# Kernel tuning notes

Hardware: AMD Instinct MI355X
Metric: run time of the kernel (lower is better)

The kernel has to match this reference:

```python
import jax, jax.numpy as jnp
import numpy as np

B, L, C = 4, 2048, 1024
H = 16
D = C // H  # head_dim = 64


def _rope(t, cos, sin):
    # t: [B, H, L, D]; cos/sin: [L, D//2] broadcast to [1, 1, L, D//2]
    te = t[..., ::2]
    to = t[..., 1::2]
    c = cos[None, None]
    s = sin[None, None]
    re = te * c - to * s
    ro = te * s + to * c
    # interleave even/odd back: [..., D//2, 2] -> [..., D]
    return jnp.stack([re, ro], axis=-1).reshape(t.shape)


def setup_inputs() -> dict:
    key = jax.random.key(0)
    ks = jax.random.split(key, 5)
    x = jax.random.normal(ks[0], (B, L, C), dtype=jnp.float32)
    # rotary phases: theta_i = 10000^(-2i/D), angles = pos * theta
    inv_freq = 1.0 / (10000.0 ** (np.arange(0, D, 2, dtype=np.float32) / D))
    ang = np.arange(L, dtype=np.float32)[:, None] * inv_freq[None, :]  # [L, D//2]
    cos = jnp.asarray(np.cos(ang))
    sin = jnp.asarray(np.sin(ang))
    w_qkv = jax.random.normal(ks[1], (3 * C, C), dtype=jnp.float32) * (C ** -0.5)
    w_proj = jax.random.normal(ks[2], (C, C), dtype=jnp.float32) * (C ** -0.5)
    b_proj = jnp.zeros((C,), dtype=jnp.float32)
    return {"x": x, "cos": cos, "sin": sin, "w_qkv": w_qkv, "w_proj": w_proj, "b_proj": b_proj}


def reference(x, cos, sin, w_qkv, w_proj, b_proj):
    Bx, Lx, Cx = x.shape
    # QKV projection (torch Linear: y = x @ W.T), then split heads
    qkv = jnp.einsum("blc,fc->blf", x, w_qkv)  # [B, L, 3C]
    qkv = qkv.reshape(Bx, Lx, 3, H, D).transpose(2, 0, 3, 1, 4)  # [3, B, H, L, D]
    q, k, v = qkv[0], qkv[1], qkv[2]
    q = _rope(q, cos, sin)
    k = _rope(k, cos, sin)
    # scaled dot-product attention, non-causal
    scale = D ** -0.5
    scores = jnp.einsum("bhqd,bhkd->bhqk", q, k) * scale
    attn = jax.nn.softmax(scores, axis=-1)
    o = jnp.einsum("bhqk,bhkd->bhqd", attn, v)  # [B, H, L, D]
    o = o.transpose(0, 2, 1, 3).reshape(Bx, Lx, Cx)
    return jnp.einsum("blc,fc->blf", o, w_proj) + b_proj
```

## Files before the change

### kernel.cpp

```cpp
#include <hip/hip_runtime.h>
#include <hip/hip_bf16.h>
#include <cstdint>


typedef unsigned short u16;
typedef __attribute__((ext_vector_type(8))) short bf16x8;
typedef __attribute__((ext_vector_type(4))) float f32x4;
typedef __attribute__((ext_vector_type(2))) unsigned int u32x2;

#define GLD16(g, l)                                                            \
  __builtin_amdgcn_global_load_lds(                                            \
      (const __attribute__((address_space(1))) void*)(g),                      \
      (__attribute__((address_space(3))) void*)(l), 16, 0, 0)

static __device__ __forceinline__ u16 f32_bf16(float f) {
  union { float f; unsigned u; } v; v.f = f;
  unsigned r = v.u + 0x7FFFu + ((v.u >> 16) & 1u);
  return (u16)(r >> 16);
}
static __device__ __forceinline__ float bf16_f32(u16 h) {
  union { unsigned u; float f; } v; v.u = ((unsigned)h) << 16;
  return v.f;
}
static __device__ __forceinline__ unsigned pack_rne(float a, float b) {
  union { float f; unsigned u; } x, y; x.f = a; y.f = b;
  unsigned ua = x.u + 0x7FFFu + ((x.u >> 16) & 1u);
  unsigned ub = y.u + 0x7FFFu + ((y.u >> 16) & 1u);
  return (ua >> 16) | (ub & 0xFFFF0000u);
}
static __device__ __forceinline__ unsigned pack_bf16_hw(float a, float b) {
  float2 t; t.x = a; t.y = b;
  __hip_bfloat162 h = __float22bfloat162_rn(t);
  union { __hip_bfloat162 h; unsigned u; } c; c.h = h;
  return c.u;
}

__global__ __launch_bounds__(256) void convert_all(
    const void* __restrict__ x, const void* __restrict__ wq,
    const void* __restrict__ wp, const void* __restrict__ cs,
    const void* __restrict__ sn, const void* __restrict__ bs,
    u16* __restrict__ xb, u16* __restrict__ wqb, u16* __restrict__ wpb,
    u16* __restrict__ cb, u16* __restrict__ sb, u16* __restrict__ bb) {
  const unsigned f32mode = (((const unsigned*)cs)[0] == 0x3F800000u);
  int blk = blockIdx.x;
  if (blk >= 12288 && blk < 12416) {
    const void* src = (blk < 12352) ? cs : sn;
    u16* dst = (blk < 12352) ? cb : sb;
    int i = (blk - ((blk < 12352) ? 12288 : 12352)) * 256 + threadIdx.x;
    u16 e[4];
    if (f32mode) {
      float4 v = ((const float4*)src)[i];
      const float* vf = (const float*)&v;
#pragma unroll
      for (int c = 0; c < 4; c++) e[c] = f32_bf16(vf[c]);
    } else {
      uint2 v = ((const uint2*)src)[i];
      e[0] = (u16)(v.x & 0xFFFFu); e[1] = (u16)(v.x >> 16);
      e[2] = (u16)(v.y & 0xFFFFu); e[3] = (u16)(v.y >> 16);
    }
#pragma unroll
    for (int c = 0; c < 4; c++) {
      int E = i * 4 + c;
      dst[(E & 31) * 2048 + (E >> 5)] = e[c];
    }
    return;
  }
  const void* src; u16* dst; int i0, n4;
  if (blk < 8192)       { src = x;  dst = xb;  i0 = blk;         n4 = 2097152; }
  else if (blk < 11264) { src = wq; dst = wqb; i0 = blk - 8192;  n4 = 786432; }
  else if (blk < 12288) { src = wp; dst = wpb; i0 = blk - 11264; n4 = 262144; }
  else                  { src = bs; dst = bb;  i0 = blk - 12416; n4 = 256; }
  int i = i0 * 256 + threadIdx.x;
  if (i >= n4) return;
  if (f32mode) {
    float4 v = ((const float4*)src)[i];
    uint2 o;
    o.x = pack_rne(v.x, v.y);
    o.y = pack_rne(v.z, v.w);
    ((uint2*)dst)[i] = o;
  } else {
    ((uint2*)dst)[i] = ((const uint2*)src)[i];
  }
}

static __device__ __forceinline__ void gemm_mainloop(
    const u16* __restrict__ A, const u16* __restrict__ Bm, int K,
    int m0, int n0, u16* As, u16* Bs, f32x4 acc[4][4]) {
  const int tid  = threadIdx.x;
  const int lane = tid & 63;
  const int wave = tid >> 6;
  const int n16  = lane & 15;
  const int quad = lane >> 4;
  const int wm = (wave >> 1) * 64;
  const int wn = (wave & 1) * 64;
  const u16* ag = A  + (size_t)(m0 + wave * 16 + (lane >> 2)) * K + (lane & 3) * 8;
  const u16* bg = Bm + (size_t)(n0 + wave * 16 + (lane >> 2)) * K + (lane & 3) * 8;
  u16* al = As + wave * (16 * 32);
  u16* bl = Bs + wave * (16 * 32);
  GLD16(ag, al);
  GLD16(ag + (size_t)64 * K, al + 64 * 32);
  GLD16(bg, bl);
  GLD16(bg + (size_t)64 * K, bl + 64 * 32);
  for (int kt = 0; kt < K; kt += 32) {
    const int buf = (kt >> 5) & 1;
    __syncthreads();
    if (kt + 32 < K) {
      const int nb = buf ^ 1;
      GLD16(ag + kt + 32, al + nb * 4096);
      GLD16(ag + (size_t)64 * K + kt + 32, al + nb * 4096 + 64 * 32);
      GLD16(bg + kt + 32, bl + nb * 4096);
      GLD16(bg + (size_t)64 * K + kt + 32, bl + nb * 4096 + 64 * 32);
    }
    const u16* as = As + buf * 4096;
    const u16* bs = Bs + buf * 4096;
    bf16x8 af[4], bf[4];
#pragma unroll
    for (int i = 0; i < 4; i++)
      af[i] = *(const bf16x8*)(as + (wm + i * 16 + n16) * 32 + quad * 8);
#pragma unroll
    for (int j = 0; j < 4; j++)
      bf[j] = *(const bf16x8*)(bs + (wn + j * 16 + n16) * 32 + quad * 8);
#pragma unroll
    for (int i = 0; i < 4; i++)
#pragma unroll
      for (int j = 0; j < 4; j++)
        acc[i][j] = __builtin_amdgcn_mfma_f32_16x16x32_bf16(af[i], bf[j], acc[i][j], 0, 0, 0);
  }
}

__global__ __launch_bounds__(256) void gemm_qkv(
    const u16* __restrict__ x, const u16* __restrict__ w,
    u16* __restrict__ q_ws, u16* __restrict__ k_ws, u16* __restrict__ vt_ws,
    const u16* __restrict__ cosT, const u16* __restrict__ sinT) {
  __shared__ u16 As[2 * 128 * 32];
  __shared__ u16 Bs[2 * 128 * 32];
  f32x4 acc[4][4];
#pragma unroll
  for (int i = 0; i < 4; i++)
#pragma unroll
    for (int j = 0; j < 4; j++) acc[i][j] = (f32x4){0.f, 0.f, 0.f, 0.f};
  const int m0 = blockIdx.y * 128;
  const int n0 = blockIdx.x * 128;
  gemm_mainloop(x, w, 1024, m0, n0, As, Bs, acc);
  const int lane = threadIdx.x & 63, wave = threadIdx.x >> 6;
  const int n16 = lane & 15, quad = lane >> 4;
  const int wm = (wave >> 1) * 64, wn = (wave & 1) * 64;
#pragma unroll
  for (int i = 0; i < 4; i++)
#pragma unroll
    for (int j = 0; j < 4; j++) {
      int f = n0 + wn + j * 16 + n16;
      int which = f >> 10;
      int rem = f & 1023;
      int h = rem >> 6, d = rem & 63;
      int l0 = m0 + wm + i * 16 + quad * 4;
      int b = l0 >> 11, l = l0 & 2047;
      if (which == 2) {
        uint2 o;
        o.x = pack_rne(acc[i][j][0], acc[i][j][1]);
        o.y = pack_rne(acc[i][j][2], acc[i][j][3]);
        size_t idx = (((size_t)b * 16 + h) * 64 + d) * 2048 + l;
        *(uint2*)(vt_ws + idx) = o;
      } else {
        u16* dst = (which == 0) ? q_ws : k_ws;
        const float sc = (which == 0) ? 0.18033688011112042f : 1.0f;
        const int ip = d >> 1;
        const bool ev = !(d & 1);
        uint2 cu = *(const uint2*)(cosT + ip * 2048 + l);
        uint2 su = *(const uint2*)(sinT + ip * 2048 + l);
        float cf[4] = {bf16_f32((u16)(cu.x & 0xFFFFu)), bf16_f32((u16)(cu.x >> 16)),
                       bf16_f32((u16)(cu.y & 0xFFFFu)), bf16_f32((u16)(cu.y >> 16))};
        float sf[4] = {bf16_f32((u16)(su.x & 0xFFFFu)), bf16_f32((u16)(su.x >> 16)),
                       bf16_f32((u16)(su.y & 0xFFFFu)), bf16_f32((u16)(su.y >> 16))};
        size_t base = (((size_t)b * 16 + h) * 2048 + l) * 64 + d;
#pragma unroll
        for (int r = 0; r < 4; r++) {
          float v = acc[i][j][r];
          float p = __shfl_xor(v, 1, 64);
          float o = ev ? (v * cf[r] - p * sf[r]) : (p * sf[r] + v * cf[r]);
          dst[base + (size_t)r * 64] = f32_bf16(o * sc);
        }
      }
    }
}

__global__ __launch_bounds__(256, 4) void flash_attn(
    const u16* __restrict__ q_ws, const u16* __restrict__ k_ws,
    const u16* __restrict__ vt_ws, u16* __restrict__ o_ws) {
  __shared__ u16 Ks[2][64 * 64];
  __shared__ u16 Vs[2][64 * 64];
  const int bh = blockIdx.x & 63;
  const int q0 = (blockIdx.x >> 6) * 128;
  const int b = bh >> 4, h = bh & 15;
  const int tid = threadIdx.x, lane = tid & 63, wave = tid >> 6;
  const int n16 = lane & 15, quad = lane >> 4;
  const int x7 = n16 & 7;
  const int pn16 = (n16 & 3) | ((n16 & 4) << 1) | ((n16 & 8) >> 1);
  const int px7 = pn16 & 7;
  const size_t hoff = (size_t)bh * (2048 * 64);

  bf16x8 qf[2][2];
#pragma unroll
  for (int qb = 0; qb < 2; qb++) {
    const u16* qrow = q_ws + hoff + (size_t)(q0 + wave * 32 + qb * 16 + n16) * 64;
    qf[qb][0] = *(const bf16x8*)(qrow + quad * 8);
    qf[qb][1] = *(const bf16x8*)(qrow + 32 + quad * 8);
  }

  f32x4 oacc[2][4];
  f32x4 lq[2];
#pragma unroll
  for (int qb = 0; qb < 2; qb++) {
    lq[qb] = (f32x4){0.f, 0.f, 0.f, 0.f};
#pragma unroll
    for (int s = 0; s < 4; s++) oacc[qb][s] = (f32x4){0.f, 0.f, 0.f, 0.f};
  }

  const int srow = wave * 8 + (lane >> 3);
  const int sw = (lane & 7) ^ ((lane >> 3) & 7);
  const u16* kg = k_ws + hoff + (size_t)srow * 64 + sw * 8;
  const u16* vg = vt_ws + hoff + (size_t)srow * 2048 + sw * 8;
  const int loff = wave * 8 * 64;

  GLD16(kg, &Ks[0][loff]);
  GLD16(kg + 32 * 64, &Ks[0][loff + 32 * 64]);
  GLD16(vg, &Vs[0][loff]);
  GLD16(vg + (size_t)32 * 2048, &Vs[0][loff + 32 * 64]);

  for (int kt = 0; kt < 2048; kt += 64) {
    const int buf = (kt >> 6) & 1;
    __syncthreads();
    if (kt + 64 < 2048) {
      const u16* kgn = kg + (size_t)(kt + 64) * 64;
      const u16* vgn = vg + (kt + 64);
      GLD16(kgn, &Ks[buf ^ 1][loff]);
      GLD16(kgn + 32 * 64, &Ks[buf ^ 1][loff + 32 * 64]);
      GLD16(vgn, &Vs[buf ^ 1][loff]);
      GLD16(vgn + (size_t)32 * 2048, &Vs[buf ^ 1][loff + 32 * 64]);
    }
    const u16* ks = Ks[buf];
    const u16* vs = Vs[buf];

    unsigned pxk[2][4], pyk[2][4];
#pragma unroll
    for (int sub = 0; sub < 4; sub++) {
      const u16* krow = ks + (sub * 16 + pn16) * 64;
      bf16x8 kf0 = *(const bf16x8*)(krow + (quad ^ px7) * 8);
      bf16x8 kf1 = *(const bf16x8*)(krow + ((quad + 4) ^ px7) * 8);
#pragma unroll
      for (int qb = 0; qb < 2; qb++) {
        f32x4 z = (f32x4){0.f, 0.f, 0.f, 0.f};
        z = __builtin_amdgcn_mfma_f32_16x16x32_bf16(kf0, qf[qb][0], z, 0, 0, 0);
        z = __builtin_amdgcn_mfma_f32_16x16x32_bf16(kf1, qf[qb][1], z, 0, 0, 0);
        f32x4 p;
#pragma unroll
        for (int r = 0; r < 4; r++) p[r] = __builtin_amdgcn_exp2f(z[r]);
        lq[qb] += p;
        pxk[qb][sub] = pack_bf16_hw(p[0], p[1]);
        pyk[qb][sub] = pack_bf16_hw(p[2], p[3]);
      }
    }

    bf16x8 pf[2][2];
#pragma unroll
    for (int qb = 0; qb < 2; qb++) {
      u32x2 r0 = __builtin_amdgcn_permlane32_swap(pxk[qb][0], pxk[qb][1], false, false);
      u32x2 r1 = __builtin_amdgcn_permlane32_swap(pyk[qb][0], pyk[qb][1], false, false);
      u32x2 r2 = __builtin_amdgcn_permlane32_swap(pxk[qb][2], pxk[qb][3], false, false);
      u32x2 r3 = __builtin_amdgcn_permlane32_swap(pyk[qb][2], pyk[qb][3], false, false);
      union { unsigned u[4]; bf16x8 v; } t0, t1;
      t0.u[0] = r0.x; t0.u[1] = r1.x; t0.u[2] = r0.y; t0.u[3] = r1.y;
      t1.u[0] = r2.x; t1.u[1] = r3.x; t1.u[2] = r2.y; t1.u[3] = r3.y;
      pf[qb][0] = t0.v;
      pf[qb][1] = t1.v;
    }

#pragma unroll
    for (int sd = 0; sd < 4; sd++) {
      const u16* vrow = vs + (sd * 16 + n16) * 64;
      bf16x8 vf0 = *(const bf16x8*)(vrow + (quad ^ x7) * 8);
      bf16x8 vf1 = *(const bf16x8*)(vrow + ((quad + 4) ^ x7) * 8);
#pragma unroll
      for (int qb = 0; qb < 2; qb++) {
        oacc[qb][sd] = __builtin_amdgcn_mfma_f32_16x16x32_bf16(pf[qb][0], vf0, oacc[qb][sd], 0, 0, 0);
        oacc[qb][sd] = __builtin_amdgcn_mfma_f32_16x16x32_bf16(pf[qb][1], vf1, oacc[qb][sd], 0, 0, 0);
      }
    }
  }

#pragma unroll
  for (int qb = 0; qb < 2; qb++) {
    float l = lq[qb][0] + lq[qb][1] + lq[qb][2] + lq[qb][3];
    l += __shfl_xor(l, 16, 64);
    l += __shfl_xor(l, 32, 64);
    float linv = 1.0f / l;
#pragma unroll
    for (int r = 0; r < 4; r++) {
      float lr = __shfl(linv, quad * 4 + r, 64);
      int row = q0 + wave * 32 + qb * 16 + quad * 4 + r;
      size_t base = ((size_t)b * 2048 + row) * 1024 + h * 64;
#pragma unroll
      for (int sd = 0; sd < 4; sd++)
        o_ws[base + sd * 16 + n16] = f32_bf16(oacc[qb][sd][r] * lr);
    }
  }
}

__global__ __launch_bounds__(256) void gemm_proj(
    const u16* __restrict__ o, const u16* __restrict__ w,
    const u16* __restrict__ bias, float* __restrict__ out) {
  __shared__ u16 As[2 * 128 * 32];
  __shared__ u16 Bs[2 * 128 * 32];
  f32x4 acc[4][4];
#pragma unroll
  for (int i = 0; i < 4; i++)
#pragma unroll
    for (int j = 0; j < 4; j++) acc[i][j] = (f32x4){0.f, 0.f, 0.f, 0.f};
  const int m0 = blockIdx.y * 128;
  const int n0 = blockIdx.x * 128;
  gemm_mainloop(o, w, 1024, m0, n0, As, Bs, acc);
  const int lane = threadIdx.x & 63, wave = threadIdx.x >> 6;
  const int n16 = lane & 15, quad = lane >> 4;
  const int wm = (wave >> 1) * 64, wn = (wave & 1) * 64;
#pragma unroll
  for (int i = 0; i < 4; i++)
#pragma unroll
    for (int j = 0; j < 4; j++) {
      int f = n0 + wn + j * 16 + n16;
      float bf = bf16_f32(bias[f]);
#pragma unroll
      for (int r = 0; r < 4; r++) {
        int m = m0 + wm + i * 16 + quad * 4 + r;
        out[(size_t)m * 1024 + f] = acc[i][j][r] + bf;
      }
    }
}

extern "C" void kernel_launch(void* const* d_in, const int* in_sizes, int n_in,
                              void* d_out, int out_size, void* d_ws, size_t ws_size,
                              hipStream_t stream) {
  float* out = (float*)d_out;

  u16* ws = (u16*)d_ws;
  u16* xb     = ws;
  u16* wqkvb  = ws + 8388608;
  u16* wprojb = ws + 11534336;
  u16* cosb   = ws + 12582912;
  u16* sinb   = ws + 12648448;
  u16* biasb  = ws + 12713984;
  u16* qb     = ws + 12715008;
  u16* kb     = ws + 21103616;
  u16* vtb    = ws + 29492224;
  u16* ob     = xb;

  convert_all<<<12417, 256, 0, stream>>>(
      d_in[0], d_in[3], d_in[4], d_in[1], d_in[2], d_in[5],
      xb, wqkvb, wprojb, cosb, sinb, biasb);

  gemm_qkv<<<dim3(24, 64), 256, 0, stream>>>(xb, wqkvb, qb, kb, vtb, cosb, sinb);
  flash_attn<<<1024, 256, 0, stream>>>(qb, kb, vtb, ob);
  gemm_proj<<<dim3(8, 64), 256, 0, stream>>>(ob, wprojb, biasb, out);
}
```

Before: 283.5 us.

## Permute QKV weight rows so RoPE pairs share a lane and drop shuffles

During bf16 conversion, the rows of the Q and K weights are reordered within each head so that even-indexed features come first and odd-indexed features second. In the GEMM epilogue each lane then holds both members of a RoPE pair in separate accumulator tiles (j and j+2). This removes the cross-lane shuffle and the even/odd branch, folds the Q scale into cos/sin, and writes packed 32-bit bf16 pairs instead of 16-bit scalars. The which/head branch is also hoisted out of the loop per wave, and a hardware pack intrinsic is used, which may round differently from the manual RNE routine.

```diff
diff --git a/kernel.cpp b/kernel.cpp
--- a/kernel.cpp
+++ b/kernel.cpp
@@ -66,20 +66,30 @@
     return;
   }
   const void* src; u16* dst; int i0, n4;
+  bool is_wq = false;
   if (blk < 8192)       { src = x;  dst = xb;  i0 = blk;         n4 = 2097152; }
-  else if (blk < 11264) { src = wq; dst = wqb; i0 = blk - 8192;  n4 = 786432; }
+  else if (blk < 11264) { src = wq; dst = wqb; i0 = blk - 8192;  n4 = 786432; is_wq = true; }
   else if (blk < 12288) { src = wp; dst = wpb; i0 = blk - 11264; n4 = 262144; }
   else                  { src = bs; dst = bb;  i0 = blk - 12416; n4 = 256; }
   int i = i0 * 256 + threadIdx.x;
   if (i >= n4) return;
+  int si = i;
+  if (is_wq) {
+    int f = i >> 8, c4 = i & 255;
+    if (f < 2048) {
+      int loc = f & 63;
+      int srcf = (f & ~63) | ((loc < 32) ? (2 * loc) : (2 * (loc - 32) + 1));
+      si = srcf * 256 + c4;
+    }
+  }
   if (f32mode) {
-    float4 v = ((const float4*)src)[i];
+    float4 v = ((const float4*)src)[si];
     uint2 o;
     o.x = pack_rne(v.x, v.y);
     o.y = pack_rne(v.z, v.w);
     ((uint2*)dst)[i] = o;
   } else {
-    ((uint2*)dst)[i] = ((const uint2*)src)[i];
+    ((uint2*)dst)[i] = ((const uint2*)src)[si];
   }
 }
 
@@ -145,43 +155,51 @@
   const int lane = threadIdx.x & 63, wave = threadIdx.x >> 6;
   const int n16 = lane & 15, quad = lane >> 4;
   const int wm = (wave >> 1) * 64, wn = (wave & 1) * 64;
-#pragma unroll
-  for (int i = 0; i < 4; i++)
-#pragma unroll
-    for (int j = 0; j < 4; j++) {
-      int f = n0 + wn + j * 16 + n16;
-      int which = f >> 10;
-      int rem = f & 1023;
-      int h = rem >> 6, d = rem & 63;
+  const int fw = n0 + wn;
+  const int which = fw >> 10;
+  const int h = (fw & 1023) >> 6;
+  if (which == 2) {
+#pragma unroll
+    for (int i = 0; i < 4; i++)
+#pragma unroll
+      for (int j = 0; j < 4; j++) {
+        int d = j * 16 + n16;
+        int l0 = m0 + wm + i * 16 + quad * 4;
+        int b = l0 >> 11, l = l0 & 2047;
+        uint2 o;
+        o.x = pack_bf16_hw(acc[i][j][0], acc[i][j][1]);
+        o.y = pack_bf16_hw(acc[i][j][2], acc[i][j][3]);
+        size_t idx = (((size_t)b * 16 + h) * 64 + d) * 2048 + l;
+        *(uint2*)(vt_ws + idx) = o;
+      }
+  } else {
+    u16* dst = (which == 0) ? q_ws : k_ws;
+    const float sc = (which == 0) ? 0.18033688011112042f : 1.0f;
+#pragma unroll
+    for (int i = 0; i < 4; i++) {
       int l0 = m0 + wm + i * 16 + quad * 4;
       int b = l0 >> 11, l = l0 & 2047;
-      if (which == 2) {
-        uint2 o;
-        o.x = pack_rne(acc[i][j][0], acc[i][j][1]);
-        o.y = pack_rne(acc[i][j][2], acc[i][j][3]);
-        size_t idx = (((size_t)b * 16 + h) * 64 + d) * 2048 + l;
-        *(uint2*)(vt_ws + idx) = o;
-      } else {
-        u16* dst = (which == 0) ? q_ws : k_ws;
-        const float sc = (which == 0) ? 0.18033688011112042f : 1.0f;
-        const int ip = d >> 1;
-        const bool ev = !(d & 1);
-        uint2 cu = *(const uint2*)(cosT + ip * 2048 + l);
-        uint2 su = *(const uint2*)(sinT + ip * 2048 + l);
-        float cf[4] = {bf16_f32((u16)(cu.x & 0xFFFFu)), bf16_f32((u16)(cu.x >> 16)),
-                       bf16_f32((u16)(cu.y & 0xFFFFu)), bf16_f32((u16)(cu.y >> 16))};
-        float sf[4] = {bf16_f32((u16)(su.x & 0xFFFFu)), bf16_f32((u16)(su.x >> 16)),
-                       bf16_f32((u16)(su.y & 0xFFFFu)), bf16_f32((u16)(su.y >> 16))};
-        size_t base = (((size_t)b * 16 + h) * 2048 + l) * 64 + d;
+#pragma unroll
+      for (int jj = 0; jj < 2; jj++) {
+        int m = jj * 16 + n16;
+        uint2 cu = *(const uint2*)(cosT + m * 2048 + l);
+        uint2 su = *(const uint2*)(sinT + m * 2048 + l);
+        float cf[4] = {bf16_f32((u16)(cu.x & 0xFFFFu)) * sc, bf16_f32((u16)(cu.x >> 16)) * sc,
+                       bf16_f32((u16)(cu.y & 0xFFFFu)) * sc, bf16_f32((u16)(cu.y >> 16)) * sc};
+        float sf[4] = {bf16_f32((u16)(su.x & 0xFFFFu)) * sc, bf16_f32((u16)(su.x >> 16)) * sc,
+                       bf16_f32((u16)(su.y & 0xFFFFu)) * sc, bf16_f32((u16)(su.y >> 16)) * sc};
+        size_t base = (((size_t)b * 16 + h) * 2048 + l) * 64 + 2 * m;
 #pragma unroll
         for (int r = 0; r < 4; r++) {
-          float v = acc[i][j][r];
-          float p = __shfl_xor(v, 1, 64);
-          float o = ev ? (v * cf[r] - p * sf[r]) : (p * sf[r] + v * cf[r]);
-          dst[base + (size_t)r * 64] = f32_bf16(o * sc);
+          float te = acc[i][jj][r];
+          float to = acc[i][jj + 2][r];
+          float re = te * cf[r] - to * sf[r];
+          float ro = te * sf[r] + to * cf[r];
+          *(unsigned*)(dst + base + (size_t)r * 64) = pack_bf16_hw(re, ro);
         }
       }
     }
+  }
 }
 
 __global__ __launch_bounds__(256, 4) void flash_attn(
```

Result: slower. 291.9 us (+3.0%).
